# Optimization experiments

Measured on AMD Instinct MI355X. Metric: run time of the kernel, lower is better.

The kernel has to match this reference:

```python
import jax, jax.numpy as jnp
import numpy as np

B, S, D, H, L, V, NP, GH = 2, 1024, 1024, 16, 6, 32000, 16, 64
DH = D // H
FF = int(D * 4 * 2 / 3)  # SwiGLU hidden = int(dim*ffn_expansion*2/3)


def setup_inputs() -> dict:
    key = jax.random.key(0)
    ks = jax.random.split(key, 12)
    n = lambda k, shp, s=0.02: (jax.random.normal(k, shp, jnp.float32) * s)
    # per-layer memory gate init: -3.0 .. -1.0 across layers
    gate_init = jnp.array([-3.0 + (i / (L - 1)) * 2.0 for i in range(L)], jnp.float32)
    return dict(
        input_ids=jax.random.randint(ks[0], (B, S), 0, V),
        tok_emb=n(ks[1], (V, D)),
        w_init=jnp.zeros((D,), jnp.float32),
        persistent=n(ks[2], (NP, D), 1.0),
        norm1_w=jnp.ones((L, D), jnp.float32),
        norm2_w=jnp.ones((L, D), jnp.float32),
        norm_f_w=jnp.ones((D,), jnp.float32),
        qkv_w=n(ks[3], (L, 3 * D, D)),
        q_norm_w=jnp.ones((L, DH), jnp.float32),
        k_norm_w=jnp.ones((L, DH), jnp.float32),
        gamma_w1=n(ks[4], (L, GH, D)),
        gamma_w2=n(ks[5], (L, 1, GH)),
        memory_gate=gate_init,
        w_o=n(ks[6], (L, D, D), 0.02 / 2 ** 0.5),
        ffn_w1=n(ks[7], (L, FF, D)),
        ffn_w2=n(ks[8], (L, FF, D)),
        ffn_w3=n(ks[9], (L, D, FF)),
    )


def _rms(x, w, eps=1e-6):
    return x * jax.lax.rsqrt(jnp.mean(x * x, axis=-1, keepdims=True) + eps) * w


def _rope_tables():
    inv_freq = 1.0 / (10000.0 ** (jnp.arange(0, DH, 2, dtype=jnp.float32) / DH))
    t = jnp.arange(S, dtype=jnp.float32)
    freqs = jnp.einsum('s,f->sf', t, inv_freq)  # (S, DH/2)
    return jnp.cos(freqs), jnp.sin(freqs)


def _rope(x, cos, sin):  # x: (B,H,S,DH)
    x1, x2 = jnp.split(x, 2, axis=-1)
    return jnp.concatenate([x1 * cos - x2 * sin, x2 * cos + x1 * sin], axis=-1)


def reference(input_ids, tok_emb, w_init, persistent, norm1_w, norm2_w, norm_f_w,
              qkv_w, q_norm_w, k_norm_w, gamma_w1, gamma_w2, memory_gate,
              w_o, ffn_w1, ffn_w2, ffn_w3):
    x = tok_emb[input_ids] + w_init  # (B,S,D)
    cos, sin = _rope_tables()
    causal = jnp.tril(jnp.ones((S, S), dtype=bool))  # True where k <= q
    scale = DH ** -0.5
    # persistent memory: per-head sum of key outer products M_p[h] = sum_j p_jh p_jh^T
    p = persistent.reshape(NP, H, DH)
    Mp = jnp.einsum('nhd,nhe->hde', p, p)
    for i in range(L):
        h = _rms(x, norm1_w[i])
        qkv = h @ qkv_w[i].T  # (B,S,3D)
        q, k, v = jnp.split(qkv, 3, axis=-1)
        q = q.reshape(B, S, H, DH).transpose(0, 2, 1, 3)
        k = k.reshape(B, S, H, DH).transpose(0, 2, 1, 3)
        v = v.reshape(B, S, H, DH).transpose(0, 2, 1, 3)
        q = _rms(q, q_norm_w[i])  # qk_norm
        k = _rms(k, k_norm_w[i])
        q = _rope(q, cos, sin)
        k = _rope(k, cos, sin)
        # gamma gate: Linear -> SiLU -> Linear -> Sigmoid, (B,S,1)
        g = jax.nn.sigmoid(jnp.einsum('oh,bsh->bso', gamma_w2[i],
                                      jax.nn.silu(jnp.einsum('hd,bsd->bsh', gamma_w1[i], h))))
        gk = g[..., 0]  # (B,S)
        # Omega-rule memory: q'_t = (M_p q_t + sum_{i<=t} gamma_i (k_i . q_t) k_i) / (NP + sum_{i<=t} gamma_i)
        mem_scores = jnp.einsum('bhqd,bhkd->bhqk', q, k) * gk[:, None, None, :]
        mem_scores = jnp.where(causal, mem_scores, 0.0)
        mem = jnp.einsum('bhqk,bhkd->bhqd', mem_scores, k)
        mpq = jnp.einsum('hde,bhse->bhsd', Mp, q)
        norm = NP + jnp.cumsum(gk, axis=1)  # (B,S)
        q_proj = (mpq + mem) / norm[:, None, :, None]
        gate = jax.nn.sigmoid(memory_gate[i])
        q = (1 - gate) * q + gate * q_proj
        # causal softmax attention
        attn = jnp.einsum('bhqd,bhkd->bhqk', q, k) * scale
        attn = jnp.where(causal, attn, jnp.finfo(attn.dtype).min)
        pw = jax.nn.softmax(attn, axis=-1)
        o = jnp.einsum('bhqk,bhkd->bhqd', pw, v).transpose(0, 2, 1, 3).reshape(B, S, D)
        x = x + o @ w_o[i].T
        # SwiGLU FFN
        h2 = _rms(x, norm2_w[i])
        x = x + (jax.nn.silu(h2 @ ffn_w1[i].T) * (h2 @ ffn_w2[i].T)) @ ffn_w3[i].T
    x = _rms(x, norm_f_w)
    return x @ tok_emb.T  # tied lm_head, (B,S,V)
```

## Files before the change

### kernel.cpp

```cpp
#include <hip/hip_runtime.h>
#include <hip/hip_bf16.h>
#include <math.h>

#define B 2
#define S 1024
#define D 1024
#define H 16
#define DH 64
#define NL 6
#define GH 64
#define NP 16
#define V 32000
#define FF 2730
#define FFP 2752
#define M (B*S)

typedef float fv4 __attribute__((ext_vector_type(4)));
typedef short bf16x8 __attribute__((ext_vector_type(8)));
typedef unsigned short us4 __attribute__((ext_vector_type(4)));
typedef unsigned short us;

#define MFMA16 __builtin_amdgcn_mfma_f32_16x16x32_bf16
#define G2L16(g, l) __builtin_amdgcn_global_load_lds( \
    (const __attribute__((address_space(1))) void*)(g), \
    (__attribute__((address_space(3))) void*)(l), 16, 0, 0)

__device__ __forceinline__ us f2bf(float f) {
  union { float f; unsigned u; } v; v.f = f;
  unsigned r = v.u + 0x7FFFu + ((v.u >> 16) & 1u);
  return (us)(r >> 16);
}
__device__ __forceinline__ float bf2f(us h) {
  union { unsigned u; float f; } v; v.u = ((unsigned)h) << 16;
  return v.f;
}

template<int N> __device__ __forceinline__ void waitcnt_vm() {
  if constexpr (N == 0)      asm volatile("s_waitcnt vmcnt(0)" ::: "memory");
  else if constexpr (N == 4) asm volatile("s_waitcnt vmcnt(4)" ::: "memory");
  else if constexpr (N == 8) asm volatile("s_waitcnt vmcnt(8)" ::: "memory");
  else if constexpr (N == 6) asm volatile("s_waitcnt vmcnt(6)" ::: "memory");
}

__device__ __forceinline__ int xcd_remap(int flat, int nwg) {
  int q = nwg >> 3, r = nwg & 7;
  int xcd = flat & 7, idx = flat >> 3;
  return (xcd < r) ? (xcd * (q + 1) + idx) : (r * (q + 1) + (xcd - r) * q + idx);
}

__global__ __launch_bounds__(256) void k_embed(const int* __restrict__ ids,
                                               const float* __restrict__ emb,
                                               const float* __restrict__ winit,
                                               float* __restrict__ x) {
  int m = blockIdx.x, t = threadIdx.x;
  int id = ids[m];
  fv4 a = *(const fv4*)(emb + (size_t)id * D + 4*t);
  fv4 w = *(const fv4*)(winit + 4*t);
  *(fv4*)(x + (size_t)m * D + 4*t) = a + w;
}

__global__ void k_rope_tables(float* __restrict__ cosT, float* __restrict__ sinT) {
  int idx = blockIdx.x * blockDim.x + threadIdx.x;
  if (idx >= S * 32) return;
  int s = idx >> 5, f = idx & 31;
  float inv = powf(10000.0f, -2.0f * (float)f / (float)DH);
  float ang = (float)s * inv;
  cosT[idx] = cosf(ang);
  sinT[idx] = sinf(ang);
}

__global__ __launch_bounds__(256) void k_mp(const float* __restrict__ pers,
                                            us* __restrict__ Mp) {
  int h = blockIdx.x, t = threadIdx.x;
  __shared__ float p[NP][DH];
  for (int i = t; i < NP * DH; i += 256) {
    int n = i / DH, dh = i % DH;
    p[n][dh] = pers[(size_t)n * D + h * DH + dh];
  }
  __syncthreads();
  for (int i = t; i < DH * DH; i += 256) {
    int d = i / DH, e = i % DH;
    float s = 0.f;
#pragma unroll
    for (int n = 0; n < NP; n++) s += p[n][d] * p[n][e];
    Mp[(size_t)h * DH * DH + i] = f2bf(s);
  }
}

__global__ __launch_bounds__(256) void k_rms(const float* __restrict__ in,
                                             const float* __restrict__ w,
                                             us* __restrict__ outb) {
  int m = blockIdx.x, t = threadIdx.x;
  fv4 v = *(const fv4*)(in + (size_t)m * D + 4*t);
  float ss = v[0]*v[0] + v[1]*v[1] + v[2]*v[2] + v[3]*v[3];
#pragma unroll
  for (int off = 32; off > 0; off >>= 1) ss += __shfl_down(ss, off);
  __shared__ float buf[4];
  if ((t & 63) == 0) buf[t >> 6] = ss;
  __syncthreads();
  float tot = buf[0] + buf[1] + buf[2] + buf[3];
  float r = rsqrtf(tot * (1.0f / (float)D) + 1e-6f);
  fv4 wv = *(const fv4*)(w + 4*t);
  fv4 res = v * r * wv;
  us4 o; o[0]=f2bf(res[0]); o[1]=f2bf(res[1]); o[2]=f2bf(res[2]); o[3]=f2bf(res[3]);
  *(us4*)(outb + (size_t)m * D + 4*t) = o;
}

__global__ __launch_bounds__(256) void k_rmsg(const float* __restrict__ in,
                                              const float* __restrict__ w,
                                              const float* __restrict__ w1,
                                              const float* __restrict__ w2,
                                              us* __restrict__ outb,
                                              float* __restrict__ gko) {
  int m = blockIdx.x, t = threadIdx.x;
  __shared__ float hrow[D];
  __shared__ float buf[4];
  __shared__ float part[4][64];
  fv4 v = *(const fv4*)(in + (size_t)m * D + 4*t);
  float ss = v[0]*v[0] + v[1]*v[1] + v[2]*v[2] + v[3]*v[3];
#pragma unroll
  for (int off = 32; off > 0; off >>= 1) ss += __shfl_down(ss, off);
  if ((t & 63) == 0) buf[t >> 6] = ss;
  __syncthreads();
  float tot = buf[0] + buf[1] + buf[2] + buf[3];
  float r = rsqrtf(tot * (1.0f / (float)D) + 1e-6f);
  fv4 wv = *(const fv4*)(w + 4*t);
  fv4 res = v * r * wv;
  us4 o; o[0]=f2bf(res[0]); o[1]=f2bf(res[1]); o[2]=f2bf(res[2]); o[3]=f2bf(res[3]);
  *(us4*)(outb + (size_t)m * D + 4*t) = o;
  *(fv4*)&hrow[4*t] = res;
  __syncthreads();
  int oo = t & 63, seg = t >> 6;
  const float* wr = w1 + (size_t)oo * D + seg * 256;
  const float* hr = hrow + seg * 256;
  float acc = 0.f;
  for (int j = 0; j < 256; j += 4) {
    fv4 wv4 = *(const fv4*)(wr + j);
    acc += wv4[0]*hr[j] + wv4[1]*hr[j+1] + wv4[2]*hr[j+2] + wv4[3]*hr[j+3];
  }
  part[seg][oo] = acc;
  __syncthreads();
  if (t < 64) {
    float dot = part[0][t] + part[1][t] + part[2][t] + part[3][t];
    float sv = dot / (1.f + expf(-dot));
    float val = sv * w2[t];
#pragma unroll
    for (int off = 32; off > 0; off >>= 1) val += __shfl_down(val, off);
    if (t == 0) gko[m] = 1.f / (1.f + expf(-val));
  }
}

__global__ __launch_bounds__(256) void k_cvt(const float* __restrict__ src,
                                             us* __restrict__ dst, int n) {
  for (size_t i = ((size_t)blockIdx.x * 256 + threadIdx.x) * 4; i < (size_t)n;
       i += (size_t)gridDim.x * 1024) {
    fv4 v = *(const fv4*)(src + i);
    us4 o; o[0]=f2bf(v[0]); o[1]=f2bf(v[1]); o[2]=f2bf(v[2]); o[3]=f2bf(v[3]);
    *(us4*)(dst + i) = o;
  }
}

#define CVT_N1 786432
#define CVT_N2 262144
#define CVT_N3 698880
#define CVT_N4 698880
#define CVT_N5 704512
__global__ __launch_bounds__(256) void k_cvtw(const float* __restrict__ s1,
                                              const float* __restrict__ s2,
                                              const float* __restrict__ s3,
                                              const float* __restrict__ s4,
                                              const float* __restrict__ s5,
                                              us* __restrict__ d1, us* __restrict__ d2,
                                              us* __restrict__ d3, us* __restrict__ d4,
                                              us* __restrict__ d5) {
  const int TOT = CVT_N1 + CVT_N2 + CVT_N3 + CVT_N4 + CVT_N5;
  for (int i = blockIdx.x * 256 + threadIdx.x; i < TOT; i += gridDim.x * 256) {
    const float* s; us* d; int j = i;
    if (j < CVT_N1) { s = s1; d = d1; }
    else if ((j -= CVT_N1) < CVT_N2) { s = s2; d = d2; }
    else if ((j -= CVT_N2) < CVT_N3) { s = s3; d = d3; }
    else if ((j -= CVT_N3) < CVT_N4) { s = s4; d = d4; }
    else {
      j -= CVT_N4;
      int r = j / (FFP/4), c = (j % (FFP/4)) * 4;
      us4 o;
#pragma unroll
      for (int q = 0; q < 4; q++) {
        int cc = c + q;
        o[q] = (cc < FF) ? f2bf(s5[(size_t)r * FF + cc]) : (us)0;
      }
      *(us4*)&d5[(size_t)r * FFP + c] = o;
      continue;
    }
    fv4 v = *(const fv4*)(s + (size_t)4 * j);
    us4 o; o[0]=f2bf(v[0]); o[1]=f2bf(v[1]); o[2]=f2bf(v[2]); o[3]=f2bf(v[3]);
    *(us4*)&d[(size_t)4 * j] = o;
  }
}

template<int ACW, int BCW>
__device__ __forceinline__ void pg_stage(const us* __restrict__ A,
                                         const us* __restrict__ W,
                                         us* bufA, us* bufB,
                                         int m0, int n0, int Nn, int Kk,
                                         int tile, int w, int lane, int lr, int sx) {
#pragma unroll
  for (int i = 0; i < ACW; i++) {
    int chunk = w * ACW + i;
    G2L16(A + (size_t)(m0 + chunk*8 + lr) * Kk + tile*64 + sx, bufA + chunk*512 + lane*8);
  }
#pragma unroll
  for (int i = 0; i < BCW; i++) {
    int chunk = w * BCW + i;
    int wrow = n0 + chunk*8 + lr;
    if (wrow >= Nn) wrow = Nn - 1;
    G2L16(W + (size_t)wrow * Kk + tile*64 + sx, bufB + chunk*512 + lane*8);
  }
}

template<int EPI, int BM, int BN>
__global__ __launch_bounds__(256) void k_pgemm(const us* __restrict__ A,
                                               const us* __restrict__ W,
                                               float* __restrict__ C,
                                               int Nn, int Kk) {
  constexpr int FM = BM / 32, FN = BN / 32;
  constexpr int ACW = BM / 32, BCW = BN / 32;
  constexpr int L = ACW + BCW;
  __shared__ __attribute__((aligned(16))) us lds[2][(BM + BN) * 64];
  int t = threadIdx.x, lane = t & 63, w = t >> 6;
  int l16 = lane & 15, lkb = lane >> 4, lr = lane >> 3;
  int sx = ((lane & 7) ^ lr) * 8;
  int sw = l16 & 7;
  int gx = gridDim.x, nwg = gx * gridDim.y;
  int nf = xcd_remap(blockIdx.y * gx + blockIdx.x, nwg);
  int m0 = (nf % gx) * BM, n0 = (nf / gx) * BN;
  int wr = w >> 1, wc = w & 1;
  int NK = Kk >> 6;

  pg_stage<ACW,BCW>(A, W, lds[0], lds[0] + BM*64, m0, n0, Nn, Kk, 0, w, lane, lr, sx);
  pg_stage<ACW,BCW>(A, W, lds[1], lds[1] + BM*64, m0, n0, Nn, Kk, 1, w, lane, lr, sx);

  fv4 acc[FM][FN] = {};
  for (int T = 0; T < NK; T++) {
    if (T == NK - 1) waitcnt_vm<0>(); else waitcnt_vm<L>();
    __builtin_amdgcn_s_barrier();
    const us* bufA = lds[T & 1];
    const us* bufB = bufA + BM*64;
    bf16x8 af[2][FM], bfh[2][FN];
#pragma unroll
    for (int kk = 0; kk < 2; kk++) {
#pragma unroll
      for (int i = 0; i < FM; i++)
        af[kk][i] = *(const bf16x8*)&bufA[(wr*(BM/2) + i*16 + l16)*64 + (((kk*4+lkb)) ^ sw)*8];
#pragma unroll
      for (int j = 0; j < FN; j++)
        bfh[kk][j] = *(const bf16x8*)&bufB[(wc*(BN/2) + j*16 + l16)*64 + (((kk*4+lkb)) ^ sw)*8];
    }
    __builtin_amdgcn_s_barrier();
    if (T + 2 < NK)
      pg_stage<ACW,BCW>(A, W, lds[T & 1], lds[T & 1] + BM*64, m0, n0, Nn, Kk, T + 2, w, lane, lr, sx);
    __builtin_amdgcn_s_setprio(1);
#pragma unroll
    for (int kk = 0; kk < 2; kk++)
#pragma unroll
      for (int i = 0; i < FM; i++)
#pragma unroll
        for (int j = 0; j < FN; j++)
          acc[i][j] = MFMA16(af[kk][i], bfh[kk][j], acc[i][j], 0, 0, 0);
    __builtin_amdgcn_s_setprio(0);
  }

#pragma unroll
  for (int i = 0; i < FM; i++) {
    int gr0 = m0 + wr*(BM/2) + i*16 + lkb*4;
#pragma unroll
    for (int j = 0; j < FN; j++) {
      int gc = n0 + wc*(BN/2) + j*16 + l16;
      if (gc < Nn) {
#pragma unroll
        for (int r = 0; r < 4; r++) {
          size_t idx = (size_t)(gr0 + r) * Nn + gc;
          float val = acc[i][j][r];
          if (EPI == 0) C[idx] = val;
          else C[idx] += val;
        }
      }
    }
  }
}

__device__ __forceinline__ void pf_stage(const us* __restrict__ A,
                                         const us* __restrict__ W1,
                                         const us* __restrict__ W2,
                                         us* buf, int m0, int n0, int Nn, int Kk,
                                         int tile, int w, int lane, int lr, int sx) {
#pragma unroll
  for (int i = 0; i < 4; i++) {
    int chunk = w * 4 + i;
    G2L16(A + (size_t)(m0 + chunk*8 + lr) * Kk + tile*64 + sx, buf + chunk*512 + lane*8);
  }
#pragma unroll
  for (int i = 0; i < 2; i++) {
    int chunk = w * 2 + i;
    int wrow = n0 + chunk*8 + lr;
    if (wrow >= Nn) wrow = Nn - 1;
    G2L16(W1 + (size_t)wrow * Kk + tile*64 + sx, buf + 8192 + chunk*512 + lane*8);
    G2L16(W2 + (size_t)wrow * Kk + tile*64 + sx, buf + 12288 + chunk*512 + lane*8);
  }
}

__global__ __launch_bounds__(256) void k_pffn12(const us* __restrict__ A,
                                                const us* __restrict__ W1,
                                                const us* __restrict__ W2,
                                                us* __restrict__ Cb,
                                                int Nn, int Kk) {
  __shared__ __attribute__((aligned(16))) us lds[2][16384];
  int t = threadIdx.x, lane = t & 63, w = t >> 6;
  int l16 = lane & 15, lkb = lane >> 4, lr = lane >> 3;
  int sx = ((lane & 7) ^ lr) * 8;
  int sw = l16 & 7;
  int gx = gridDim.x, nwg = gx * gridDim.y;
  int nf = xcd_remap(blockIdx.y * gx + blockIdx.x, nwg);
  int m0 = (nf % gx) * 128, n0 = (nf / gx) * 64;
  int wr = w >> 1, wc = w & 1;
  int NK = Kk >> 6;

  pf_stage(A, W1, W2, lds[0], m0, n0, Nn, Kk, 0, w, lane, lr, sx);
  pf_stage(A, W1, W2, lds[1], m0, n0, Nn, Kk, 1, w, lane, lr, sx);

  fv4 acc1[4][2] = {}, acc2[4][2] = {};
  for (int T = 0; T < NK; T++) {
    if (T == NK - 1) waitcnt_vm<0>(); else waitcnt_vm<8>();
    __builtin_amdgcn_s_barrier();
    const us* buf = lds[T & 1];
    bf16x8 af[2][4], b1f[2][2], b2f[2][2];
#pragma unroll
    for (int kk = 0; kk < 2; kk++) {
#pragma unroll
      for (int i = 0; i < 4; i++)
        af[kk][i] = *(const bf16x8*)&buf[(wr*64 + i*16 + l16)*64 + ((kk*4+lkb) ^ sw)*8];
#pragma unroll
      for (int j = 0; j < 2; j++) {
        b1f[kk][j] = *(const bf16x8*)&buf[8192  + (wc*32 + j*16 + l16)*64 + ((kk*4+lkb) ^ sw)*8];
        b2f[kk][j] = *(const bf16x8*)&buf[12288 + (wc*32 + j*16 + l16)*64 + ((kk*4+lkb) ^ sw)*8];
      }
    }
    __builtin_amdgcn_s_barrier();
    if (T + 2 < NK)
      pf_stage(A, W1, W2, lds[T & 1], m0, n0, Nn, Kk, T + 2, w, lane, lr, sx);
    __builtin_amdgcn_s_setprio(1);
#pragma unroll
    for (int kk = 0; kk < 2; kk++)
#pragma unroll
      for (int i = 0; i < 4; i++)
#pragma unroll
        for (int j = 0; j < 2; j++) {
          acc1[i][j] = MFMA16(af[kk][i], b1f[kk][j], acc1[i][j], 0, 0, 0);
          acc2[i][j] = MFMA16(af[kk][i], b2f[kk][j], acc2[i][j], 0, 0, 0);
        }
    __builtin_amdgcn_s_setprio(0);
  }

#pragma unroll
  for (int i = 0; i < 4; i++) {
    int gr0 = m0 + wr*64 + i*16 + lkb*4;
#pragma unroll
    for (int j = 0; j < 2; j++) {
      int gc = n0 + wc*32 + j*16 + l16;
      if (gc < Nn) {
#pragma unroll
        for (int r = 0; r < 4; r++) {
          float v1 = acc1[i][j][r], v2 = acc2[i][j][r];
          float sv = v1 / (1.f + expf(-v1));
          Cb[(size_t)(gr0 + r) * FFP + gc] = f2bf(sv * v2);
        }
      }
    }
  }
}

__global__ __launch_bounds__(256) void k_pqkv(const us* __restrict__ A,
                                              const us* __restrict__ W,
                                              const float* __restrict__ qnw,
                                              const float* __restrict__ knw,
                                              const float* __restrict__ cosT,
                                              const float* __restrict__ sinT,
                                              us* __restrict__ qb,
                                              us* __restrict__ kb,
                                              us* __restrict__ vb) {
  const int Kk = D, Nn = 3 * D;
  __shared__ __attribute__((aligned(16))) us lds[2][16384];
  int t = threadIdx.x, lane = t & 63, w = t >> 6;
  int l16 = lane & 15, lkb = lane >> 4, lr = lane >> 3;
  int sx = ((lane & 7) ^ lr) * 8;
  int sw = l16 & 7;
  int gx = gridDim.x, nwg = gx * gridDim.y;
  int nf = xcd_remap(blockIdx.y * gx + blockIdx.x, nwg);
  int m0 = (nf % gx) * 128, n0 = (nf / gx) * 128;
  int wr = w >> 1, wc = w & 1;
  int NK = Kk >> 6;

  pg_stage<4,4>(A, W, lds[0], lds[0] + 8192, m0, n0, Nn, Kk, 0, w, lane, lr, sx);
  pg_stage<4,4>(A, W, lds[1], lds[1] + 8192, m0, n0, Nn, Kk, 1, w, lane, lr, sx);

  fv4 acc[4][4] = {};
  for (int T = 0; T < NK; T++) {
    if (T == NK - 1) waitcnt_vm<0>(); else waitcnt_vm<8>();
    __builtin_amdgcn_s_barrier();
    const us* bufA = lds[T & 1];
    const us* bufB = bufA + 8192;
    bf16x8 af[2][4], bfh[2][4];
#pragma unroll
    for (int kk = 0; kk < 2; kk++) {
#pragma unroll
      for (int i = 0; i < 4; i++) {
        af[kk][i]  = *(const bf16x8*)&bufA[(wr*64 + i*16 + l16)*64 + ((kk*4+lkb) ^ sw)*8];
        bfh[kk][i] = *(const bf16x8*)&bufB[(wc*64 + i*16 + l16)*64 + ((kk*4+lkb) ^ sw)*8];
      }
    }
    __builtin_amdgcn_s_barrier();
    if (T + 2 < NK)
      pg_stage<4,4>(A, W, lds[T & 1], lds[T & 1] + 8192, m0, n0, Nn, Kk, T + 2, w, lane, lr, sx);
    __builtin_amdgcn_s_setprio(1);
#pragma unroll
    for (int kk = 0; kk < 2; kk++)
#pragma unroll
      for (int i = 0; i < 4; i++)
#pragma unroll
        for (int j = 0; j < 4; j++)
          acc[i][j] = MFMA16(af[kk][i], bfh[kk][j], acc[i][j], 0, 0, 0);
    __builtin_amdgcn_s_setprio(0);
  }

  int part = n0 >> 10;
  int hd = ((n0 & 1023) + wc * 64) >> 6;
  us* dst = (part == 0) ? qb : ((part == 1) ? kb : vb);
  if (part == 2) {
#pragma unroll
    for (int i = 0; i < 4; i++)
#pragma unroll
      for (int r = 0; r < 4; r++) {
        int m = m0 + wr*64 + i*16 + lkb*4 + r;
        int b = m >> 10, s = m & 1023;
        us* drow = dst + (((size_t)(b*H + hd)) * S + s) * 64;
#pragma unroll
        for (int j = 0; j < 4; j++) drow[j*16 + l16] = f2bf(acc[i][j][r]);
      }
  } else {
    const float* nw = (part == 0) ? qnw : knw;
    float w0 = nw[l16], w1 = nw[16 + l16], w2 = nw[32 + l16], w3 = nw[48 + l16];
#pragma unroll
    for (int i = 0; i < 4; i++)
#pragma unroll
      for (int r = 0; r < 4; r++) {
        int m = m0 + wr*64 + i*16 + lkb*4 + r;
        int b = m >> 10, s = m & 1023;
        float a0 = acc[i][0][r], a1 = acc[i][1][r], a2 = acc[i][2][r], a3 = acc[i][3][r];
        float s2 = a0*a0 + a1*a1 + a2*a2 + a3*a3;
        s2 += __shfl_xor(s2, 1); s2 += __shfl_xor(s2, 2);
        s2 += __shfl_xor(s2, 4); s2 += __shfl_xor(s2, 8);
        float rs = rsqrtf(s2 * (1.0f / (float)DH) + 1e-6f);
        float v0 = a0 * rs * w0, v1 = a1 * rs * w1, v2 = a2 * rs * w2, v3 = a3 * rs * w3;
        float c0 = cosT[s*32 + l16],      sn0 = sinT[s*32 + l16];
        float c1 = cosT[s*32 + 16 + l16], sn1 = sinT[s*32 + 16 + l16];
        us* drow = dst + (((size_t)(b*H + hd)) * S + s) * 64;
        drow[l16]      = f2bf(v0 * c0 - v2 * sn0);
        drow[16 + l16] = f2bf(v1 * c1 - v3 * sn1);
        drow[32 + l16] = f2bf(v2 * c0 + v0 * sn0);
        drow[48 + l16] = f2bf(v3 * c1 + v1 * sn1);
      }
  }
}

struct G8 { const us* A; const us* W; int K; int m0; int n0; };

__device__ __forceinline__ void g8_issue(const G8& g, us* lds8, int q, int t) {
  int tile = q >> 2, h = q & 3;
  us* buf = lds8 + (size_t)(tile & 1) * 32768;
  const us* Gp = (h < 2) ? g.A : g.W;
  int rbase = ((h < 2) ? g.m0 : g.n0) + (h & 1) * 128;
  us* part = buf + (h >> 1) * 16384 + (h & 1) * 8192;
  int r8 = t >> 3;
  int sl = (((t & 7) ^ (r8 & 7)) * 8);
#pragma unroll
  for (int c = 0; c < 2; c++) {
    const us* src = Gp + (size_t)(rbase + c * 64 + r8) * g.K + tile * 64 + sl;
    us* dst = part + c * 4096 + t * 8;
    G2L16(src, dst);
  }
}

__global__ __launch_bounds__(512, 2) void k_gemm8(const us* __restrict__ A,
                                                  const us* __restrict__ W,
                                                  float* __restrict__ C,
                                                  int Nn, int Kk) {
  __shared__ __attribute__((aligned(16))) us lds8[65536];
  int t = threadIdx.x, lane = t & 63, w = t >> 6;
  int wm = w >> 2, wn = w & 3;
  int l16 = lane & 15, lkb = lane >> 4;
  int gx = gridDim.x, nwg = gx * gridDim.y;
  int nf = xcd_remap(blockIdx.y * gx + blockIdx.x, nwg);
  int m0 = (nf % gx) * 256, n0 = (nf / gx) * 256;
  G8 g{A, W, Kk, m0, n0};
  int NK = Kk >> 6, QMAX = NK * 4;

  int q = 0;
  for (; q < 7 && q < QMAX; ++q) g8_issue(g, lds8, q, t);

  fv4 acc[8][4] = {};
  int arow = wm * 128 + l16;
  int brow = wn * 64 + l16;
  int sw = l16 & 7;

  for (int T = 0; T < NK; ++T) {
    if (q < QMAX) { g8_issue(g, lds8, q, t); q++; }
    if (T == NK - 1) asm volatile("s_waitcnt vmcnt(0)" ::: "memory");
    else             asm volatile("s_waitcnt vmcnt(8)" ::: "memory");
    __builtin_amdgcn_s_barrier();
    const us* buf = lds8 + (size_t)(T & 1) * 32768;
    bf16x8 a0[8], a1[8], b0[4], b1[4];
#pragma unroll
    for (int i = 0; i < 8; i++) {
      a0[i] = *(const bf16x8*)&buf[(arow + i*16)*64 + ((lkb     ) ^ sw)*8];
      a1[i] = *(const bf16x8*)&buf[(arow + i*16)*64 + ((lkb +  4) ^ sw)*8];
    }
#pragma unroll
    for (int j = 0; j < 4; j++) {
      b0[j] = *(const bf16x8*)&buf[16384 + (brow + j*16)*64 + ((lkb    ) ^ sw)*8];
      b1[j] = *(const bf16x8*)&buf[16384 + (brow + j*16)*64 + ((lkb + 4) ^ sw)*8];
    }
    __builtin_amdgcn_s_barrier();
    __builtin_amdgcn_s_setprio(1);
#pragma unroll
    for (int i = 0; i < 8; i++)
#pragma unroll
      for (int j = 0; j < 4; j++)
        acc[i][j] = MFMA16(a0[i], b0[j], acc[i][j], 0, 0, 0);
    __builtin_amdgcn_s_setprio(0);
    if (q < QMAX) { g8_issue(g, lds8, q, t); q++; }
    if (q < QMAX) { g8_issue(g, lds8, q, t); q++; }
    if (q < QMAX) { g8_issue(g, lds8, q, t); q++; }
    __builtin_amdgcn_s_setprio(1);
#pragma unroll
    for (int i = 0; i < 8; i++)
#pragma unroll
      for (int j = 0; j < 4; j++)
        acc[i][j] = MFMA16(a1[i], b1[j], acc[i][j], 0, 0, 0);
    __builtin_amdgcn_s_setprio(0);
  }

#pragma unroll
  for (int i = 0; i < 8; i++) {
    int gr0 = m0 + wm*128 + i*16 + lkb*4;
#pragma unroll
    for (int j = 0; j < 4; j++) {
      int gc = n0 + wn*64 + j*16 + l16;
#pragma unroll
      for (int r = 0; r < 4; r++)
        C[(size_t)(gr0 + r) * Nn + gc] = acc[i][j][r];
    }
  }
}

__global__ __launch_bounds__(256) void k_tr2(const us* __restrict__ ksrc,
                                             const us* __restrict__ vsrc,
                                             us* __restrict__ kdst,
                                             us* __restrict__ vdst) {
  __shared__ __attribute__((aligned(16))) us tile[64*72];
  int st = blockIdx.x, bh = blockIdx.y, t = threadIdx.x;
  const us* src = blockIdx.z ? vsrc : ksrc;
  us* dst = blockIdx.z ? vdst : kdst;
  const us* sp = src + ((size_t)bh * S + st*64) * 64;
#pragma unroll
  for (int p = 0; p < 2; p++) {
    int idx = t + p*256;
    int r = idx >> 3, c = (idx & 7)*8;
    *(bf16x8*)&tile[r*72 + c] = *(const bf16x8*)&sp[(size_t)idx*8];
  }
  __syncthreads();
  int d = t >> 2;
#pragma unroll
  for (int cc = 0; cc < 16; cc += 8) {
    int s0 = (t & 3)*16 + cc;
    bf16x8 vv;
#pragma unroll
    for (int j2 = 0; j2 < 8; j2++) vv[j2] = (short)tile[(s0+j2)*72 + d];
    *(bf16x8*)&dst[((size_t)bh*64 + d)*S + st*64 + s0] = vv;
  }
}

#define SM_OFF 24.0f

__device__ __forceinline__ void m_stage(const us* __restrict__ src, int rstride,
                                        us* buf, int w, int lane, int lr, int sx8) {
#pragma unroll
  for (int i = 0; i < 2; i++) {
    int rbase = i * 32 + w * 8;
    G2L16(src + (size_t)(rbase + lr) * rstride + sx8, buf + rbase * 64 + lane * 8);
  }
}

__global__ __launch_bounds__(256) void k_matt(const us* __restrict__ qb,
                                              const us* __restrict__ kb,
                                              const us* __restrict__ kbT,
                                              const us* __restrict__ vbT,
                                              const us* __restrict__ MpB,
                                              const float* __restrict__ gk,
                                              const float* __restrict__ mg, int layer,
                                              us* __restrict__ ob) {
  int nf = xcd_remap(blockIdx.y * 8 + blockIdx.x, 256);
  int xx = nf & 7, bh = nf >> 3;
  int b = bh >> 4, hh = bh & 15;
  int t = threadIdx.x, lane = t & 63, w = t >> 6;
  int l16 = lane & 15, lg = lane >> 4, lr = lane >> 3;
  int sx8 = ((lane & 7) ^ lr) * 8;
  int sw = l16 & 7;

  __shared__ __attribute__((aligned(16))) us Qs[64*72];
  __shared__ __attribute__((aligned(16))) us Ms[64*72];
  __shared__ __attribute__((aligned(16))) us Ps[64*72];
  __shared__ __attribute__((aligned(16))) us KT[2][2][64*64];
  __shared__ float gkL[S], nrmL[S];
  __shared__ float wsum2[4];

  float gate = 1.f / (1.f + expf(-mg[layer]));
  const us* kbB = kb + (size_t)bh * S * 64;
  const us* ktB = kbT + (size_t)bh * 64 * S;
  const us* vtB = vbT + (size_t)bh * 64 * S;

  {
    const us* mp = MpB + (size_t)hh * 4096;
#pragma unroll
    for (int p = 0; p < 2; p++) {
      int idx = t + p*256;
      int r = idx >> 3, c = (idx & 7) * 8;
      *(bf16x8*)&Ms[r*72 + c] = *(const bf16x8*)&mp[(size_t)idx*8];
    }
#pragma unroll
    for (int p = 0; p < 4; p++) gkL[t + p*256] = gk[b*S + t + p*256];
  }
  __syncthreads();
  {
    float v0 = gkL[4*t], v1 = gkL[4*t+1], v2 = gkL[4*t+2], v3 = gkL[4*t+3];
    float r0 = v0, r1 = r0 + v1, r2 = r1 + v2, r3 = r2 + v3;
    float s = r3;
#pragma unroll
    for (int off = 1; off < 64; off <<= 1) {
      float y = __shfl_up(s, off, 64);
      if (lane >= off) s += y;
    }
    if (lane == 63) wsum2[w] = s;
    __syncthreads();
    float wexcl = 0.f;
    if (w == 1) wexcl = wsum2[0];
    else if (w == 2) wexcl = wsum2[0] + wsum2[1];
    else if (w == 3) wexcl = wsum2[0] + wsum2[1] + wsum2[2];
    float base = wexcl + (s - r3);
    nrmL[4*t]   = (float)NP + base + r0;
    nrmL[4*t+1] = (float)NP + base + r1;
    nrmL[4*t+2] = (float)NP + base + r2;
    nrmL[4*t+3] = (float)NP + base + r3;
  }

  for (int sel = 0; sel < 2; sel++) {
    int qt = sel ? (15 - xx) : xx;
    __syncthreads();
    {
      const us* src = qb + ((size_t)bh * S + qt*64) * 64;
#pragma unroll
      for (int p = 0; p < 2; p++) {
        int idx = t + p*256;
        int r = idx >> 3, c = (idx & 7) * 8;
        *(bf16x8*)&Qs[r*72 + c] = *(const bf16x8*)&src[(size_t)idx*8];
      }
    }
    __syncthreads();

    bf16x8 aq0 = *(const bf16x8*)&Qs[(16*w + l16)*72 + lg*8];
    bf16x8 aq1 = *(const bf16x8*)&Qs[(16*w + l16)*72 + 32 + lg*8];

    fv4 am[4];
#pragma unroll
    for (int j = 0; j < 4; j++) {
      bf16x8 b0 = *(const bf16x8*)&Ms[(16*j + l16)*72 + lg*8];
      bf16x8 b1 = *(const bf16x8*)&Ms[(16*j + l16)*72 + 32 + lg*8];
      fv4 z = {};
      z = MFMA16(aq0, b0, z, 0, 0, 0);
      z = MFMA16(aq1, b1, z, 0, 0, 0);
      am[j] = z;
    }

    m_stage(kbB,            64, KT[0][0], w, lane, lr, sx8);
    m_stage(ktB,            S,  KT[0][1], w, lane, lr, sx8);
    m_stage(kbB + 4096,     64, KT[1][0], w, lane, lr, sx8);
    m_stage(ktB + 64,       S,  KT[1][1], w, lane, lr, sx8);
    for (int kt = 0; kt <= qt; kt++) {
      int ks = kt * 64;
      if (kt == qt) waitcnt_vm<0>(); else waitcnt_vm<4>();
      __builtin_amdgcn_s_barrier();
      const us* bK = KT[kt & 1][0];
      const us* bT = KT[kt & 1][1];
      bf16x8 kf0[4], kf1[4], tf0[4], tf1[4];
      float gv[4];
#pragma unroll
      for (int j = 0; j < 4; j++) {
        int row = 16*j + l16;
        kf0[j] = *(const bf16x8*)&bK[row*64 + ((lg    ) ^ sw)*8];
        kf1[j] = *(const bf16x8*)&bK[row*64 + ((lg + 4) ^ sw)*8];
        tf0[j] = *(const bf16x8*)&bT[row*64 + ((lg    ) ^ sw)*8];
        tf1[j] = *(const bf16x8*)&bT[row*64 + ((lg + 4) ^ sw)*8];
        gv[j] = gkL[ks + row];
      }
      __builtin_amdgcn_s_barrier();
      if (kt + 2 <= qt) {
        m_stage(kbB + (size_t)(kt+2)*4096, 64, KT[kt & 1][0], w, lane, lr, sx8);
        m_stage(ktB + (kt+2)*64,           S,  KT[kt & 1][1], w, lane, lr, sx8);
      }
      fv4 sc[4];
      __builtin_amdgcn_s_setprio(1);
#pragma unroll
      for (int j = 0; j < 4; j++) {
        fv4 z = {};
        z = MFMA16(aq0, kf0[j], z, 0, 0, 0);
        z = MFMA16(aq1, kf1[j], z, 0, 0, 0);
        sc[j] = z;
      }
      __builtin_amdgcn_s_setprio(0);
      if (kt < qt) {
#pragma unroll
        for (int j = 0; j < 4; j++)
#pragma unroll
          for (int r = 0; r < 4; r++)
            Ps[(16*w + lg*4 + r)*72 + 16*j + l16] = f2bf(sc[j][r] * gv[j]);
      } else {
#pragma unroll
        for (int j = 0; j < 4; j++) {
          int kj = 16*j + l16;
#pragma unroll
          for (int r = 0; r < 4; r++) {
            int qi = 16*w + lg*4 + r;
            Ps[qi*72 + kj] = (kj > qi) ? (us)0 : f2bf(sc[j][r] * gv[j]);
          }
        }
      }
      bf16x8 ap0 = *(const bf16x8*)&Ps[(16*w + l16)*72 + lg*8];
      bf16x8 ap1 = *(const bf16x8*)&Ps[(16*w + l16)*72 + 32 + lg*8];
      __builtin_amdgcn_s_setprio(1);
#pragma unroll
      for (int j = 0; j < 4; j++) {
        am[j] = MFMA16(ap0, tf0[j], am[j], 0, 0, 0);
        am[j] = MFMA16(ap1, tf1[j], am[j], 0, 0, 0);
      }
      __builtin_amdgcn_s_setprio(0);
    }

#pragma unroll
    for (int j = 0; j < 4; j++)
#pragma unroll
      for (int r = 0; r < 4; r++) {
        int qi = 16*w + lg*4 + r, dj = 16*j + l16;
        float qold = bf2f(Qs[qi*72 + dj]);
        float qn = (1.f - gate) * qold + gate * (am[j][r] / nrmL[qt*64 + qi]);
        Qs[qi*72 + dj] = f2bf(qn);
      }
    aq0 = *(const bf16x8*)&Qs[(16*w + l16)*72 + lg*8];
    aq1 = *(const bf16x8*)&Qs[(16*w + l16)*72 + 32 + lg*8];

    float lsum[4] = {};
    fv4 ao[4] = {};
    m_stage(kbB,            64, KT[0][0], w, lane, lr, sx8);
    m_stage(vtB,            S,  KT[0][1], w, lane, lr, sx8);
    m_stage(kbB + 4096,     64, KT[1][0], w, lane, lr, sx8);
    m_stage(vtB + 64,       S,  KT[1][1], w, lane, lr, sx8);
    for (int kt = 0; kt <= qt; kt++) {
      if (kt == qt) waitcnt_vm<0>(); else waitcnt_vm<4>();
      __builtin_amdgcn_s_barrier();
      const us* bK = KT[kt & 1][0];
      const us* bV = KT[kt & 1][1];
      bf16x8 kf0[4], kf1[4], vf0[4], vf1[4];
#pragma unroll
      for (int j = 0; j < 4; j++) {
        int row = 16*j + l16;
        kf0[j] = *(const bf16x8*)&bK[row*64 + ((lg    ) ^ sw)*8];
        kf1[j] = *(const bf16x8*)&bK[row*64 + ((lg + 4) ^ sw)*8];
        vf0[j] = *(const bf16x8*)&bV[row*64 + ((lg    ) ^ sw)*8];
        vf1[j] = *(const bf16x8*)&bV[row*64 + ((lg + 4) ^ sw)*8];
      }
      __builtin_amdgcn_s_barrier();
      if (kt + 2 <= qt) {
        m_stage(kbB + (size_t)(kt+2)*4096, 64, KT[kt & 1][0], w, lane, lr, sx8);
        m_stage(vtB + (kt+2)*64,           S,  KT[kt & 1][1], w, lane, lr, sx8);
      }
      fv4 sc[4];
      __builtin_amdgcn_s_setprio(1);
#pragma unroll
      for (int j = 0; j < 4; j++) {
        fv4 z = {};
        z = MFMA16(aq0, kf0[j], z, 0, 0, 0);
        z = MFMA16(aq1, kf1[j], z, 0, 0, 0);
        sc[j] = z;
      }
      __builtin_amdgcn_s_setprio(0);
      if (kt < qt) {
#pragma unroll
        for (int j = 0; j < 4; j++)
#pragma unroll
          for (int r = 0; r < 4; r++) {
            float p = __expf(fmaf(sc[j][r], 0.125f, -SM_OFF));
            lsum[r] += p;
            Ps[(16*w + lg*4 + r)*72 + 16*j + l16] = f2bf(p);
          }
      } else {
#pragma unroll
        for (int j = 0; j < 4; j++) {
          int kj = 16*j + l16;
#pragma unroll
          for (int r = 0; r < 4; r++) {
            int qi = 16*w + lg*4 + r;
            float p = (kj > qi) ? 0.f : __expf(fmaf(sc[j][r], 0.125f, -SM_OFF));
            lsum[r] += p;
            Ps[qi*72 + kj] = f2bf(p);
          }
        }
      }
      bf16x8 ap0 = *(const bf16x8*)&Ps[(16*w + l16)*72 + lg*8];
      bf16x8 ap1 = *(const bf16x8*)&Ps[(16*w + l16)*72 + 32 + lg*8];
      __builtin_amdgcn_s_setprio(1);
#pragma unroll
      for (int j = 0; j < 4; j++) {
        ao[j] = MFMA16(ap0, vf0[j], ao[j], 0, 0, 0);
        ao[j] = MFMA16(ap1, vf1[j], ao[j], 0, 0, 0);
      }
      __builtin_amdgcn_s_setprio(0);
    }

#pragma unroll
    for (int r = 0; r < 4; r++) {
      float l = lsum[r];
      l += __shfl_xor(l, 1);
      l += __shfl_xor(l, 2);
      l += __shfl_xor(l, 4);
      l += __shfl_xor(l, 8);
      lsum[r] = l;
    }
#pragma unroll
    for (int j = 0; j < 4; j++)
#pragma unroll
      for (int r = 0; r < 4; r++) {
        int qi = 16*w + lg*4 + r;
        ob[((size_t)b*S + qt*64 + qi) * D + hh*64 + 16*j + l16] = f2bf(ao[j][r] / lsum[r]);
      }
  }
}

extern "C" void kernel_launch(void* const* d_in, const int* in_sizes, int n_in,
                              void* d_out, int out_size, void* d_ws, size_t ws_size,
                              hipStream_t stream) {
  const int*   ids      = (const int*)d_in[0];
  const float* tok_emb  = (const float*)d_in[1];
  const float* w_init   = (const float*)d_in[2];
  const float* persist  = (const float*)d_in[3];
  const float* norm1_w  = (const float*)d_in[4];
  const float* norm2_w  = (const float*)d_in[5];
  const float* norm_f_w = (const float*)d_in[6];
  const float* qkv_w    = (const float*)d_in[7];
  const float* q_norm_w = (const float*)d_in[8];
  const float* k_norm_w = (const float*)d_in[9];
  const float* gamma_w1 = (const float*)d_in[10];
  const float* gamma_w2 = (const float*)d_in[11];
  const float* mem_gate = (const float*)d_in[12];
  const float* w_o      = (const float*)d_in[13];
  const float* ffn_w1   = (const float*)d_in[14];
  const float* ffn_w2   = (const float*)d_in[15];
  const float* ffn_w3   = (const float*)d_in[16];
  float* out = (float*)d_out;

  float* ws   = (float*)d_ws;
  float* x    = ws;
  us*    hbf  = (us*)(x + 2097152);
  float* gk   = x + 2097152 + 1048576;
  float* nrm  = gk + 2048;
  float* cosT = nrm + 2048;
  float* sinT = cosT + 32768;
  us*    MpBH = (us*)(sinT + 32768);
  float* h    = sinT + 32768 + 65536;
  float* qkv  = h + 2097152;
  us*    obf  = (us*)(qkv + 6291456);
  us*    qb   = obf + 2097152;
  us*    kb   = qb + 2097152;
  us*    vb   = kb + 2097152;
  us*    kbT  = vb + 2097152;
  us*    vbT  = kbT + 2097152;
  us*    f1bf = vbT + 2097152;
  us*    wq   = f1bf + (size_t)M*FFP;
  us*    wo   = wq + 3145728;
  us*    w1c  = wo + 1048576;
  us*    w2c  = w1c + 2795520;
  us*    w3c  = w2c + 2795520;
  us*    temb = (us*)h;

  k_embed<<<M, 256, 0, stream>>>(ids, tok_emb, w_init, x);
  k_rope_tables<<<(S*32 + 255)/256, 256, 0, stream>>>(cosT, sinT);
  k_mp<<<H, 256, 0, stream>>>(persist, MpBH);

  for (int l = 0; l < NL; l++) {
    k_cvtw<<<2048, 256, 0, stream>>>(qkv_w + (size_t)l*3*D*D, w_o + (size_t)l*D*D,
                                     ffn_w1 + (size_t)l*FF*D, ffn_w2 + (size_t)l*FF*D,
                                     ffn_w3 + (size_t)l*D*FF,
                                     wq, wo, w1c, w2c, w3c);
    k_rmsg<<<M, 256, 0, stream>>>(x, norm1_w + (size_t)l * D,
                                  gamma_w1 + (size_t)l*GH*D, gamma_w2 + (size_t)l*GH,
                                  hbf, gk);
    k_pqkv<<<dim3(16, 24), 256, 0, stream>>>(hbf, wq,
                                             q_norm_w + (size_t)l*DH, k_norm_w + (size_t)l*DH,
                                             cosT, sinT, qb, kb, vb);
    k_tr2<<<dim3(S/64, B*H, 2), 256, 0, stream>>>(kb, vb, kbT, vbT);
    k_matt<<<dim3(8, B*H), 256, 0, stream>>>(qb, kb, kbT, vbT, MpBH, gk, mem_gate, l, obf);
    k_pgemm<2,64,64><<<dim3(M/64, D/64), 256, 0, stream>>>(obf, wo, x, D, D);
    k_rms<<<M, 256, 0, stream>>>(x, norm2_w + (size_t)l * D, hbf);
    k_pffn12<<<dim3(M/128, (FF+63)/64), 256, 0, stream>>>(hbf, w1c, w2c, f1bf, FF, D);
    k_pgemm<2,64,64><<<dim3(M/64, D/64), 256, 0, stream>>>(f1bf, w3c, x, D, FFP);
  }

  k_rms<<<M, 256, 0, stream>>>(x, norm_f_w, hbf);
  k_cvt<<<2048, 256, 0, stream>>>(tok_emb, temb, V*D);
  k_gemm8<<<dim3(8, V/256), 512, 0, stream>>>(hbf, temb, out, V, D);
}
```

Baseline: 1.419 ms.

## Restructure GEMM main loop into four fragment-interleaved MFMA phases with one-tile prefetch

The 256x256 GEMM kernel no longer loads every A/B LDS fragment for a K-tile up front. It now loads them in four smaller chunks, each followed by its MFMA block, so fewer fragment registers are live at once. The global-to-LDS prefetch is simplified to exactly the next tile, issued in two halves between MFMA phases. Each iteration now waits with vmcnt(0) and uses a single barrier. This trades the previous deeper prefetch (about seven quarters ahead) and its partial waitcnt for lower register pressure and fewer barriers, at the risk of exposing more global-load latency.

New measurement: 1.406 ms. No clear change (-0.9%).

```diff
diff --git a/kernel.cpp b/kernel.cpp
--- a/kernel.cpp
+++ b/kernel.cpp
@@ -502,10 +502,10 @@
   int nf = xcd_remap(blockIdx.y * gx + blockIdx.x, nwg);
   int m0 = (nf % gx) * 256, n0 = (nf / gx) * 256;
   G8 g{A, W, Kk, m0, n0};
-  int NK = Kk >> 6, QMAX = NK * 4;
-
-  int q = 0;
-  for (; q < 7 && q < QMAX; ++q) g8_issue(g, lds8, q, t);
+  int NK = Kk >> 6;
+
+#pragma unroll
+  for (int q = 0; q < 4; ++q) g8_issue(g, lds8, q, t);
 
   fv4 acc[8][4] = {};
   int arow = wm * 128 + l16;
@@ -513,39 +513,63 @@
   int sw = l16 & 7;
 
   for (int T = 0; T < NK; ++T) {
-    if (q < QMAX) { g8_issue(g, lds8, q, t); q++; }
-    if (T == NK - 1) asm volatile("s_waitcnt vmcnt(0)" ::: "memory");
-    else             asm volatile("s_waitcnt vmcnt(8)" ::: "memory");
+    waitcnt_vm<0>();
     __builtin_amdgcn_s_barrier();
     const us* buf = lds8 + (size_t)(T & 1) * 32768;
-    bf16x8 a0[8], a1[8], b0[4], b1[4];
-#pragma unroll
-    for (int i = 0; i < 8; i++) {
-      a0[i] = *(const bf16x8*)&buf[(arow + i*16)*64 + ((lkb     ) ^ sw)*8];
-      a1[i] = *(const bf16x8*)&buf[(arow + i*16)*64 + ((lkb +  4) ^ sw)*8];
-    }
-#pragma unroll
-    for (int j = 0; j < 4; j++) {
-      b0[j] = *(const bf16x8*)&buf[16384 + (brow + j*16)*64 + ((lkb    ) ^ sw)*8];
-      b1[j] = *(const bf16x8*)&buf[16384 + (brow + j*16)*64 + ((lkb + 4) ^ sw)*8];
-    }
-    __builtin_amdgcn_s_barrier();
+    bool pf = (T + 1 < NK);
+    int qb = (T + 1) * 4;
+    bf16x8 a[4], bfr[4];
+
+#pragma unroll
+    for (int j = 0; j < 4; j++)
+      bfr[j] = *(const bf16x8*)&buf[16384 + (brow + j*16)*64 + ((lkb    ) ^ sw)*8];
+#pragma unroll
+    for (int i = 0; i < 4; i++)
+      a[i] = *(const bf16x8*)&buf[(arow + i*16)*64 + ((lkb    ) ^ sw)*8];
+    if (pf) { g8_issue(g, lds8, qb + 0, t); g8_issue(g, lds8, qb + 1, t); }
     __builtin_amdgcn_s_setprio(1);
 #pragma unroll
-    for (int i = 0; i < 8; i++)
+    for (int i = 0; i < 4; i++)
 #pragma unroll
       for (int j = 0; j < 4; j++)
-        acc[i][j] = MFMA16(a0[i], b0[j], acc[i][j], 0, 0, 0);
+        acc[i][j] = MFMA16(a[i], bfr[j], acc[i][j], 0, 0, 0);
     __builtin_amdgcn_s_setprio(0);
-    if (q < QMAX) { g8_issue(g, lds8, q, t); q++; }
-    if (q < QMAX) { g8_issue(g, lds8, q, t); q++; }
-    if (q < QMAX) { g8_issue(g, lds8, q, t); q++; }
+
+#pragma unroll
+    for (int i = 0; i < 4; i++)
+      a[i] = *(const bf16x8*)&buf[(arow + (i+4)*16)*64 + ((lkb    ) ^ sw)*8];
+    if (pf) { g8_issue(g, lds8, qb + 2, t); g8_issue(g, lds8, qb + 3, t); }
     __builtin_amdgcn_s_setprio(1);
 #pragma unroll
-    for (int i = 0; i < 8; i++)
+    for (int i = 0; i < 4; i++)
 #pragma unroll
       for (int j = 0; j < 4; j++)
-        acc[i][j] = MFMA16(a1[i], b1[j], acc[i][j], 0, 0, 0);
+        acc[i+4][j] = MFMA16(a[i], bfr[j], acc[i+4][j], 0, 0, 0);
+    __builtin_amdgcn_s_setprio(0);
+
+#pragma unroll
+    for (int j = 0; j < 4; j++)
+      bfr[j] = *(const bf16x8*)&buf[16384 + (brow + j*16)*64 + ((lkb + 4) ^ sw)*8];
+#pragma unroll
+    for (int i = 0; i < 4; i++)
+      a[i] = *(const bf16x8*)&buf[(arow + i*16)*64 + ((lkb + 4) ^ sw)*8];
+    __builtin_amdgcn_s_setprio(1);
+#pragma unroll
+    for (int i = 0; i < 4; i++)
+#pragma unroll
+      for (int j = 0; j < 4; j++)
+        acc[i][j] = MFMA16(a[i], bfr[j], acc[i][j], 0, 0, 0);
+    __builtin_amdgcn_s_setprio(0);
+
+#pragma unroll
+    for (int i = 0; i < 4; i++)
+      a[i] = *(const bf16x8*)&buf[(arow + (i+4)*16)*64 + ((lkb + 4) ^ sw)*8];
+    __builtin_amdgcn_s_setprio(1);
+#pragma unroll
+    for (int i = 0; i < 4; i++)
+#pragma unroll
+      for (int j = 0; j < 4; j++)
+        acc[i+4][j] = MFMA16(a[i], bfr[j], acc[i+4][j], 0, 0, 0);
     __builtin_amdgcn_s_setprio(0);
   }
 
```
